# Performance work log

Hardware: AMD Instinct MI355X
Metric: run time of the kernel (lower is better)

Reference implementation:

```python
import jax, jax.numpy as jnp
import numpy as np

B, S, D = 4, 2048, 1024

def setup_inputs() -> dict:
    key = jax.random.key(0)
    ks = jax.random.split(key, 7)
    s = 1.0 / np.sqrt(D)
    return {
        "x": jax.random.normal(ks[0], (B, S, D), dtype=jnp.float32),
        "Wk": jax.random.uniform(ks[1], (D, D), jnp.float32, -s, s),
        "bk": jax.random.uniform(ks[2], (D,), jnp.float32, -s, s),
        "Wq": jax.random.uniform(ks[3], (D, D), jnp.float32, -s, s),
        "bq": jax.random.uniform(ks[4], (D,), jnp.float32, -s, s),
        "Wv": jax.random.uniform(ks[5], (D, D), jnp.float32, -s, s),
        "bv": jax.random.uniform(ks[6], (D,), jnp.float32, -s, s),
    }

def reference(x, Wk, bk, Wq, bq, Wv, bv):
    # Linear projections (torch Linear: x @ W.T + b; here weights stored as [in, out])
    k = jnp.einsum('bsd,de->bse', x, Wk) + bk
    q = jnp.einsum('bsd,de->bse', x, Wq) + bq
    v = jnp.einsum('bsd,de->bse', x, Wv) + bv
    scale = jnp.asarray(q.shape[-1], q.dtype) ** 0.5
    scores = jnp.einsum('bqd,bkd->bqk', q, k) / scale  # [B,S,S]
    attn = jax.nn.softmax(scores, axis=-1)
    y = jnp.einsum('bqk,bkd->bqd', attn, v)
    return y
```

## Files before the change

### kernel.cpp

```cpp
#include <hip/hip_runtime.h>
#include <hip/hip_bf16.h>


typedef __attribute__((ext_vector_type(8))) short short8;
typedef __attribute__((ext_vector_type(4))) float f32x4;

__device__ __forceinline__ unsigned short f2b(float f) {
    unsigned u = __builtin_bit_cast(unsigned, f);
    unsigned r = 0x7FFFu + ((u >> 16) & 1u);
    return (unsigned short)((u + r) >> 16);
}
__device__ __forceinline__ float b2f(unsigned short h) {
    return __builtin_bit_cast(float, ((unsigned)h) << 16);
}

__device__ __forceinline__ void gload16(const void* g, void* lds_uniform_base) {
    __builtin_amdgcn_global_load_lds(
        (const __attribute__((address_space(1))) unsigned int*)(unsigned long long)g,
        (__attribute__((address_space(3))) unsigned int*)(unsigned)(unsigned long long)lds_uniform_base,
        16, 0, 0);
}

#define BARRIER __builtin_amdgcn_s_barrier()
#define WAIT_LGKM0 do { asm volatile("s_waitcnt lgkmcnt(0)" ::: "memory"); __builtin_amdgcn_sched_barrier(0); } while (0)
#define WAIT_VM(n) do { asm volatile("s_waitcnt vmcnt(" #n ")" ::: "memory"); __builtin_amdgcn_sched_barrier(0); } while (0)

__global__ void cvt_x(const float* __restrict__ x, unsigned short* __restrict__ xb) {
    int i = blockIdx.x * 256 + threadIdx.x;
    float4 v = ((const float4*)x)[i];
    ushort4 o;
    o.x = f2b(v.x); o.y = f2b(v.y); o.z = f2b(v.z); o.w = f2b(v.w);
    ((ushort4*)xb)[i] = o;
}

__global__ void transpose_w(const float* __restrict__ w0, const float* __restrict__ w1,
                            const float* __restrict__ w2, unsigned short* __restrict__ wt) {
    const float* W = (blockIdx.z == 0) ? w0 : (blockIdx.z == 1) ? w1 : w2;
    __shared__ float t[32][33];
    int k0 = blockIdx.y * 32, n0 = blockIdx.x * 32;
    int tx = threadIdx.x, ty = threadIdx.y;
#pragma unroll
    for (int i = 0; i < 4; i++)
        t[ty * 4 + i][tx] = W[(size_t)(k0 + ty * 4 + i) * 1024 + n0 + tx];
    __syncthreads();
    unsigned short* out = wt + (size_t)blockIdx.z * 1024 * 1024;
#pragma unroll
    for (int i = 0; i < 4; i++)
        out[(size_t)(n0 + ty * 4 + i) * 1024 + k0 + tx] = f2b(t[tx][ty * 4 + i]);
}

template <int MODE>
__global__ __launch_bounds__(512, 2) void gemm8(
    const unsigned short* __restrict__ A, const unsigned short* __restrict__ Bm,
    void* __restrict__ C0, void* __restrict__ C1, void* __restrict__ C2,
    const float* __restrict__ bias0, const float* __restrict__ bias1,
    const float* __restrict__ bias2,
    int N, int K, long long sA, long long sB, long long sC, float alpha) {
    __shared__ unsigned short As[2][256 * 64];
    __shared__ unsigned short Bs[2][256 * 64];
    const int tid = threadIdx.x;
    const int wave = tid >> 6, lane = tid & 63;

    const int gx = gridDim.x, gy = gridDim.y;
    const int nwg = gx * gy * (int)gridDim.z;
    const int orig = blockIdx.x + gx * (blockIdx.y + gy * blockIdx.z);
    const int q8 = nwg >> 3, r8 = nwg & 7;
    const int xcd = orig & 7, sub = orig >> 3;
    const int wg = (xcd < r8 ? xcd * (q8 + 1) : r8 * (q8 + 1) + (xcd - r8) * q8) + sub;
    const int bx = wg % gx;
    const int tmp = wg / gx;
    const int by = tmp % gy, bz = tmp / gy;

    const int m0 = by * 256, n0 = bx * 256;
    A += (long long)bz * sA;
    Bm += (long long)bz * sB;

    const int wm = wave >> 2, wn = wave & 3;
    const int l16 = lane & 15;
    const int lk = (lane >> 4) << 3;
    const int nt = K >> 6;

    f32x4 acc[8][4];
#pragma unroll
    for (int m = 0; m < 8; m++)
#pragma unroll
        for (int n = 0; n < 4; n++) acc[m][n] = (f32x4){0.f, 0.f, 0.f, 0.f};

    const int strow = tid >> 3;
    const int stkk = (tid & 7) << 3;

    auto ST_A = [&](int bb, int c, int tt) {
        if (tt >= nt) return;
        gload16(A + (size_t)(m0 + c * 64 + strow) * K + (tt << 6) + stkk,
                (char*)&As[bb][0] + c * 8192 + wave * 1024);
    };
    auto ST_B = [&](int bb, int c, int tt) {
        if (tt >= nt) return;
        gload16(Bm + (size_t)(n0 + c * 64 + strow) * K + (tt << 6) + stkk,
                (char*)&Bs[bb][0] + c * 8192 + wave * 1024);
    };

    short8 af[4][2], bf0[2][2], bf1[2][2];
    auto DS_A = [&](int bb, int mh) {
#pragma unroll
        for (int fm = 0; fm < 4; fm++)
#pragma unroll
            for (int ks = 0; ks < 2; ks++)
                af[fm][ks] = *(const short8*)
                    &As[bb][(wm * 128 + mh * 64 + fm * 16 + l16) * 64 + ks * 32 + lk];
    };
    auto DS_B = [&](int bb, int nh, short8 (&bf)[2][2]) {
#pragma unroll
        for (int fn = 0; fn < 2; fn++)
#pragma unroll
            for (int ks = 0; ks < 2; ks++)
                bf[fn][ks] = *(const short8*)
                    &Bs[bb][(wn * 64 + nh * 32 + fn * 16 + l16) * 64 + ks * 32 + lk];
    };
    auto MFMA16 = [&](int mh, int nh, short8 (&bf)[2][2]) {
        __builtin_amdgcn_s_setprio(1);
#pragma unroll
        for (int fm = 0; fm < 4; fm++)
#pragma unroll
            for (int fn = 0; fn < 2; fn++)
#pragma unroll
                for (int ks = 0; ks < 2; ks++)
                    acc[mh * 4 + fm][nh * 2 + fn] = __builtin_amdgcn_mfma_f32_16x16x32_bf16(
                        af[fm][ks], bf[fn][ks], acc[mh * 4 + fm][nh * 2 + fn], 0, 0, 0);
        __builtin_amdgcn_s_setprio(0);
    };

    ST_A(0, 0, 0); ST_A(0, 1, 0); ST_A(0, 2, 0); ST_A(0, 3, 0);
    ST_B(0, 0, 0); ST_B(0, 1, 0); ST_B(0, 2, 0); ST_B(0, 3, 0);
    ST_A(1, 0, 1); ST_A(1, 1, 1); ST_A(1, 2, 1); ST_A(1, 3, 1);
    ST_B(1, 0, 1); ST_B(1, 1, 1);
    WAIT_VM(6);
    BARRIER;

    for (int it = 0; it < (nt >> 1); ++it) {
        const int t = it << 1;
        const bool last = (t + 2 >= nt);
        DS_A(0, 0); DS_B(0, 0, bf0);
        ST_B(1, 2, t + 1); ST_B(1, 3, t + 1);
        BARRIER; WAIT_LGKM0;
        MFMA16(0, 0, bf0);
        BARRIER;
        DS_B(0, 1, bf1);
        ST_A(0, 0, t + 2); ST_A(0, 2, t + 2);
        BARRIER; WAIT_LGKM0;
        MFMA16(0, 1, bf1);
        BARRIER;
        DS_A(0, 1);
        ST_B(0, 0, t + 2); ST_B(0, 1, t + 2);
        BARRIER; WAIT_LGKM0;
        MFMA16(1, 0, bf0);
        BARRIER;
        ST_A(0, 1, t + 2); ST_A(0, 3, t + 2);
        BARRIER;
        MFMA16(1, 1, bf1);
        if (last) { WAIT_VM(0); } else { WAIT_VM(6); }
        BARRIER;
        DS_A(1, 0); DS_B(1, 0, bf0);
        ST_B(0, 2, t + 2); ST_B(0, 3, t + 2);
        BARRIER; WAIT_LGKM0;
        MFMA16(0, 0, bf0);
        BARRIER;
        DS_B(1, 1, bf1);
        ST_A(1, 0, t + 3); ST_A(1, 2, t + 3);
        BARRIER; WAIT_LGKM0;
        MFMA16(0, 1, bf1);
        BARRIER;
        DS_A(1, 1);
        ST_B(1, 0, t + 3); ST_B(1, 1, t + 3);
        BARRIER; WAIT_LGKM0;
        MFMA16(1, 0, bf0);
        BARRIER;
        ST_A(1, 1, t + 3); ST_A(1, 3, t + 3);
        BARRIER;
        MFMA16(1, 1, bf1);
        if (last) { WAIT_VM(0); } else { WAIT_VM(6); }
        BARRIER;
    }

    const int rowb0 = m0 + wm * 128 + ((lane >> 4) << 2);
#pragma unroll
    for (int m = 0; m < 8; m++) {
#pragma unroll
        for (int n = 0; n < 4; n++) {
            const int row = rowb0 + m * 16;
            const int col = n0 + wn * 64 + n * 16 + l16;
            if (MODE == 0) {
                unsigned short* C = (unsigned short*)C0 + (long long)bz * sC;
                float bb = bias0 ? bias0[col] : 0.f;
#pragma unroll
                for (int i = 0; i < 4; i++)
                    C[(size_t)(row + i) * N + col] = f2b(acc[m][n][i] * alpha + bb);
            } else if (MODE == 2) {
                float* C = (float*)C0 + (long long)bz * sC;
                float bb = bias0 ? bias0[col] : 0.f;
#pragma unroll
                for (int i = 0; i < 4; i++)
                    C[(size_t)(row + i) * N + col] = acc[m][n][i] * alpha + bb;
            } else {
                const int sel = col >> 10, lc = col & 1023;
                const float bb = (sel == 0 ? bias0 : sel == 1 ? bias1 : bias2)[lc];
                if (sel < 2) {
                    unsigned short* C = (unsigned short*)(sel == 0 ? C0 : C1);
#pragma unroll
                    for (int i = 0; i < 4; i++)
                        C[(size_t)(row + i) * 1024 + lc] = f2b(acc[m][n][i] + bb);
                } else {
                    const int b = row >> 11, s = row & 2047;
                    ushort4 pk;
                    pk.x = f2b(acc[m][n][0] + bb);
                    pk.y = f2b(acc[m][n][1] + bb);
                    pk.z = f2b(acc[m][n][2] + bb);
                    pk.w = f2b(acc[m][n][3] + bb);
                    *(ushort4*)((unsigned short*)C2 + (size_t)b * 2097152 +
                                (size_t)lc * 2048 + s) = pk;
                }
            }
        }
    }
}

__global__ __launch_bounds__(256) void softmax_inplace(unsigned short* __restrict__ sc) {
    const size_t row = blockIdx.x;
    unsigned short* p = sc + row * 2048;
    const int tid = threadIdx.x;
    const int wave = tid >> 6, lane = tid & 63;
    short8 raw = *(const short8*)&p[tid * 8];
    float f[8];
#pragma unroll
    for (int i = 0; i < 8; i++) f[i] = b2f((unsigned short)raw[i]);
    float mx = f[0];
#pragma unroll
    for (int i = 1; i < 8; i++) mx = fmaxf(mx, f[i]);
#pragma unroll
    for (int o = 32; o > 0; o >>= 1) mx = fmaxf(mx, __shfl_xor(mx, o, 64));
    __shared__ float red[8];
    if (lane == 0) red[wave] = mx;
    __syncthreads();
    mx = fmaxf(fmaxf(red[0], red[1]), fmaxf(red[2], red[3]));
    float e[8], s = 0.f;
#pragma unroll
    for (int i = 0; i < 8; i++) { e[i] = __expf(f[i] - mx); s += e[i]; }
#pragma unroll
    for (int o = 32; o > 0; o >>= 1) s += __shfl_xor(s, o, 64);
    if (lane == 0) red[4 + wave] = s;
    __syncthreads();
    s = (red[4] + red[5]) + (red[6] + red[7]);
    float r = 1.0f / s;
    short8 outv;
#pragma unroll
    for (int i = 0; i < 8; i++) outv[i] = (short)f2b(e[i] * r);
    *(short8*)&p[tid * 8] = outv;
}

extern "C" void kernel_launch(void* const* d_in, const int* in_sizes, int n_in,
                              void* d_out, int out_size, void* d_ws, size_t ws_size,
                              hipStream_t stream) {
    const float* x  = (const float*)d_in[0];
    const float* Wk = (const float*)d_in[1];
    const float* bk = (const float*)d_in[2];
    const float* Wq = (const float*)d_in[3];
    const float* bq = (const float*)d_in[4];
    const float* Wv = (const float*)d_in[5];
    const float* bv = (const float*)d_in[6];
    float* out = (float*)d_out;

    char* ws = (char*)d_ws;
    unsigned short* xb  = (unsigned short*)(ws);
    unsigned short* wt  = (unsigned short*)(ws + 16777216);
    unsigned short* kb  = (unsigned short*)(ws + 23068672);
    unsigned short* qb  = (unsigned short*)(ws + 39845888);
    unsigned short* vtb = (unsigned short*)(ws + 56623104);
    unsigned short* sc  = (unsigned short*)(ws + 73400320);

    cvt_x<<<8192, 256, 0, stream>>>(x, xb);
    transpose_w<<<dim3(32, 32, 3), dim3(32, 8), 0, stream>>>(Wk, Wq, Wv, wt);

    gemm8<3><<<dim3(12, 32, 1), 512, 0, stream>>>(
        xb, wt, kb, qb, vtb, bk, bq, bv, 3072, 1024, 0, 0, 0, 1.f);

    gemm8<0><<<dim3(8, 8, 4), 512, 0, stream>>>(
        qb, kb, sc, nullptr, nullptr, nullptr, nullptr, nullptr,
        2048, 1024, 2048LL * 1024, 2048LL * 1024, 2048LL * 2048, 0.03125f);

    softmax_inplace<<<8192, 256, 0, stream>>>(sc);

    gemm8<2><<<dim3(4, 8, 4), 512, 0, stream>>>(
        sc, vtb, out, nullptr, nullptr, nullptr, nullptr, nullptr,
        1024, 2048, 2048LL * 2048, 1024LL * 2048, 2048LL * 1024, 1.f);
}
```

Measured before the change: 326.2 us.

## Swizzle LDS layout in gemm8 and use smaller-tile gemm for PV

Applies an XOR swizzle to the LDS column offsets in gemm8, both when staging and when reading fragments, to reduce LDS bank conflicts. It also removes the sched_barrier from the wait macros and adds a partial lgkmcnt wait. The final attention-times-V GEMM moves to a new simpler double-buffered kernel with 256x128 tiles, doubling the workgroup count for that GEMM. In exchange the new kernel has a simpler, less overlapped pipeline, and dropping the sched barriers gives the compiler more freedom to reorder around the waits.

```diff
diff --git a/kernel.cpp b/kernel.cpp
--- a/kernel.cpp
+++ b/kernel.cpp
@@ -22,8 +22,9 @@
 }
 
 #define BARRIER __builtin_amdgcn_s_barrier()
-#define WAIT_LGKM0 do { asm volatile("s_waitcnt lgkmcnt(0)" ::: "memory"); __builtin_amdgcn_sched_barrier(0); } while (0)
-#define WAIT_VM(n) do { asm volatile("s_waitcnt vmcnt(" #n ")" ::: "memory"); __builtin_amdgcn_sched_barrier(0); } while (0)
+#define WAIT_LGKM0 asm volatile("s_waitcnt lgkmcnt(0)")
+#define WAIT_LGKM8 asm volatile("s_waitcnt lgkmcnt(8)")
+#define WAIT_VM(n) asm volatile("s_waitcnt vmcnt(" #n ")")
 
 __global__ void cvt_x(const float* __restrict__ x, unsigned short* __restrict__ xb) {
     int i = blockIdx.x * 256 + threadIdx.x;
@@ -77,7 +78,8 @@
 
     const int wm = wave >> 2, wn = wave & 3;
     const int l16 = lane & 15;
-    const int lk = (lane >> 4) << 3;
+    const int g0 = lane >> 4;
+    const int lsw = l16 & 7;
     const int nt = K >> 6;
 
     f32x4 acc[8][4];
@@ -87,7 +89,7 @@
         for (int n = 0; n < 4; n++) acc[m][n] = (f32x4){0.f, 0.f, 0.f, 0.f};
 
     const int strow = tid >> 3;
-    const int stkk = (tid & 7) << 3;
+    const int stkk = ((tid & 7) ^ (strow & 7)) << 3;
 
     auto ST_A = [&](int bb, int c, int tt) {
         if (tt >= nt) return;
@@ -107,7 +109,8 @@
 #pragma unroll
             for (int ks = 0; ks < 2; ks++)
                 af[fm][ks] = *(const short8*)
-                    &As[bb][(wm * 128 + mh * 64 + fm * 16 + l16) * 64 + ks * 32 + lk];
+                    &As[bb][(wm * 128 + mh * 64 + fm * 16 + l16) * 64 +
+                            ((((ks << 2) + g0) ^ lsw) << 3)];
     };
     auto DS_B = [&](int bb, int nh, short8 (&bf)[2][2]) {
 #pragma unroll
@@ -115,7 +118,8 @@
 #pragma unroll
             for (int ks = 0; ks < 2; ks++)
                 bf[fn][ks] = *(const short8*)
-                    &Bs[bb][(wn * 64 + nh * 32 + fn * 16 + l16) * 64 + ks * 32 + lk];
+                    &Bs[bb][(wn * 64 + nh * 32 + fn * 16 + l16) * 64 +
+                            ((((ks << 2) + g0) ^ lsw) << 3)];
     };
     auto MFMA16 = [&](int mh, int nh, short8 (&bf)[2][2]) {
         __builtin_amdgcn_s_setprio(1);
@@ -142,6 +146,7 @@
         const bool last = (t + 2 >= nt);
         DS_A(0, 0); DS_B(0, 0, bf0);
         ST_B(1, 2, t + 1); ST_B(1, 3, t + 1);
+        WAIT_LGKM8;
         BARRIER; WAIT_LGKM0;
         MFMA16(0, 0, bf0);
         BARRIER;
@@ -162,6 +167,7 @@
         BARRIER;
         DS_A(1, 0); DS_B(1, 0, bf0);
         ST_B(0, 2, t + 2); ST_B(0, 3, t + 2);
+        WAIT_LGKM8;
         BARRIER; WAIT_LGKM0;
         MFMA16(0, 0, bf0);
         BARRIER;
@@ -224,6 +230,108 @@
     }
 }
 
+template <int BN, int MODE>
+__global__ __launch_bounds__(512, 2) void gemm2(
+    const unsigned short* __restrict__ A, const unsigned short* __restrict__ Bm,
+    void* __restrict__ Cv, const float* __restrict__ bias,
+    int N, int K, long long sA, long long sB, long long sC, float alpha) {
+    constexpr int FN = BN / 64;
+    __shared__ unsigned short As[2][256 * 64];
+    __shared__ unsigned short Bs[2][BN * 64];
+    const int tid = threadIdx.x;
+    const int wave = tid >> 6, lane = tid & 63;
+
+    const int gx = gridDim.x, gy = gridDim.y;
+    const int nwg = gx * gy * (int)gridDim.z;
+    const int orig = blockIdx.x + gx * (blockIdx.y + gy * blockIdx.z);
+    const int q8 = nwg >> 3, r8 = nwg & 7;
+    const int xcd = orig & 7, sub = orig >> 3;
+    const int wg = (xcd < r8 ? xcd * (q8 + 1) : r8 * (q8 + 1) + (xcd - r8) * q8) + sub;
+    const int bx = wg % gx;
+    const int tmp = wg / gx;
+    const int by = tmp % gy, bz = tmp / gy;
+
+    const int m0 = by * 256, n0 = bx * BN;
+    A += (long long)bz * sA;
+    Bm += (long long)bz * sB;
+
+    const int wm = wave >> 2, wn = wave & 3;
+    const int l16 = lane & 15;
+    const int lk = (lane >> 4) << 3;
+
+    f32x4 acc[8][FN];
+#pragma unroll
+    for (int m = 0; m < 8; m++)
+#pragma unroll
+        for (int n = 0; n < FN; n++) acc[m][n] = (f32x4){0.f, 0.f, 0.f, 0.f};
+
+    auto STAGE = [&](int buf, int t) {
+        const int k0 = t << 6;
+#pragma unroll
+        for (int j = 0; j < 4; j++) {
+            int cid = tid + j * 512;
+            int row = cid >> 3, kk = (cid & 7) << 3;
+            gload16(A + (size_t)(m0 + row) * K + k0 + kk,
+                    (char*)&As[buf][0] + wave * 1024 + j * 8192);
+        }
+#pragma unroll
+        for (int j = 0; j < FN; j++) {
+            int cid = tid + j * 512;
+            int row = cid >> 3, kk = (cid & 7) << 3;
+            gload16(Bm + (size_t)(n0 + row) * K + k0 + kk,
+                    (char*)&Bs[buf][0] + wave * 1024 + j * 8192);
+        }
+    };
+
+    const int nt = K >> 6;
+    int cur = 0;
+    STAGE(0, 0);
+    __syncthreads();
+    for (int t = 0; t < nt; ++t) {
+        if (t + 1 < nt) STAGE(cur ^ 1, t + 1);
+#pragma unroll
+        for (int ks = 0; ks < 2; ks++) {
+            short8 af[8], bf[FN];
+#pragma unroll
+            for (int m = 0; m < 8; m++)
+                af[m] = *(const short8*)&As[cur][(wm * 128 + m * 16 + l16) * 64 + ks * 32 + lk];
+#pragma unroll
+            for (int n = 0; n < FN; n++)
+                bf[n] = *(const short8*)&Bs[cur][(wn * (BN / 4) + n * 16 + l16) * 64 + ks * 32 + lk];
+#pragma unroll
+            for (int m = 0; m < 8; m++)
+#pragma unroll
+                for (int n = 0; n < FN; n++)
+                    acc[m][n] = __builtin_amdgcn_mfma_f32_16x16x32_bf16(af[m], bf[n], acc[m][n], 0, 0, 0);
+        }
+        __syncthreads();
+        cur ^= 1;
+    }
+
+    const int rowb0 = m0 + wm * 128 + ((lane >> 4) << 2);
+    const int colb0 = n0 + wn * (BN / 4) + l16;
+#pragma unroll
+    for (int m = 0; m < 8; m++) {
+#pragma unroll
+        for (int n = 0; n < FN; n++) {
+            int col = colb0 + n * 16;
+            int rowb = rowb0 + m * 16;
+            float bv_ = bias ? bias[col] : 0.f;
+            if (MODE == 2) {
+                float* C = (float*)Cv + (long long)bz * sC;
+#pragma unroll
+                for (int i = 0; i < 4; i++)
+                    C[(size_t)(rowb + i) * N + col] = acc[m][n][i] * alpha + bv_;
+            } else {
+                unsigned short* C = (unsigned short*)Cv + (long long)bz * sC;
+#pragma unroll
+                for (int i = 0; i < 4; i++)
+                    C[(size_t)(rowb + i) * N + col] = f2b(acc[m][n][i] * alpha + bv_);
+            }
+        }
+    }
+}
+
 __global__ __launch_bounds__(256) void softmax_inplace(unsigned short* __restrict__ sc) {
     const size_t row = blockIdx.x;
     unsigned short* p = sc + row * 2048;
@@ -289,7 +397,7 @@
 
     softmax_inplace<<<8192, 256, 0, stream>>>(sc);
 
-    gemm8<2><<<dim3(4, 8, 4), 512, 0, stream>>>(
-        sc, vtb, out, nullptr, nullptr, nullptr, nullptr, nullptr,
-        1024, 2048, 2048LL * 2048, 1024LL * 2048, 2048LL * 1024, 1.f);
-}
+    gemm2<128, 2><<<dim3(8, 8, 4), 512, 0, stream>>>(
+        sc, vtb, out, nullptr, 1024, 2048,
+        2048LL * 2048, 1024LL * 2048, 2048LL * 1024, 1.f);
+}
```

Measured after the change: 266.6 us. 1.22x faster.
